# Performance work log

Measured on AMD Instinct MI355X. Metric: run time of the kernel, lower is better.

The kernel has to match this reference:

```python
import jax, jax.numpy as jnp
import numpy as np

COMMITMENT_COST = 0.25


def setup_inputs() -> dict:
    key = jax.random.key(0)
    k1, k2 = jax.random.split(key)
    B, D, H, W = 16, 256, 32, 32
    K = 8192
    z = jax.random.normal(k1, (B, D, H, W), dtype=jnp.float32)
    embeddings = jax.random.uniform(k2, (K, D), dtype=jnp.float32,
                                    minval=-1.0 / K, maxval=1.0 / K)
    return {"z": z, "embeddings": embeddings}


def reference(z, embeddings):
    B, D, H, W = z.shape
    # NCHW -> NHWC, flatten spatial+batch to code vectors [N, D]
    z_p = jnp.transpose(z, (0, 2, 3, 1))
    z_flat = z_p.reshape(-1, D)
    # squared-distance via matmul: ||z||^2 + ||e||^2 - 2 z.e^T  -> [N, K]
    d = (jnp.sum(z_flat * z_flat, axis=1, keepdims=True)
         + jnp.sum(embeddings * embeddings, axis=1)
         - 2.0 * jnp.matmul(z_flat, embeddings.T))
    encoding_indices = jnp.argmin(d, axis=1)  # [N]
    quantized = embeddings[encoding_indices].reshape(z_p.shape)  # [B,H,W,D]
    e_latent_loss = jnp.mean((jax.lax.stop_gradient(quantized) - z_p) ** 2)
    q_latent_loss = jnp.mean((quantized - jax.lax.stop_gradient(z_p)) ** 2)
    loss = q_latent_loss + COMMITMENT_COST * e_latent_loss
    # straight-through estimator
    quantized_st = z_p + jax.lax.stop_gradient(quantized - z_p)
    out = jnp.transpose(quantized_st, (0, 3, 1, 2))  # back to NCHW
    return out, loss, encoding_indices.reshape(B, H, W)
```

## Files before the change

kernel.cpp:

```cpp
#include <hip/hip_runtime.h>

#define B_    16
#define D_    256
#define H_    32
#define W_    32
#define SP    1024
#define N_TOT 16384
#define K_    8192
#define ZB    (D_*SP)

#define BIAS_  0.03125f
#define DELTA_ 2.5e-4f

typedef __attribute__((ext_vector_type(8))) short bf16x8;
typedef __attribute__((ext_vector_type(4))) short bf16x4;
typedef __attribute__((ext_vector_type(4))) float f32x4;

#define GLOAD_LDS16(g, l) \
    __builtin_amdgcn_global_load_lds((const __attribute__((address_space(1))) void*)(g), \
                                     (__attribute__((address_space(3))) void*)(l), 16, 0, 0)

__device__ __forceinline__ unsigned short f2bf(float f) {
    unsigned u = __float_as_uint(f);
    u += 0x7FFFu + ((u >> 16) & 1u);
    return (unsigned short)(u >> 16);
}

__device__ __forceinline__ void merge2(unsigned &a1, unsigned &a2,
                                       unsigned b1, unsigned b2) {
    unsigned m1  = min(a1, b1);
    unsigned hi  = max(a1, b1);
    unsigned sel = (a1 < b1) ? a2 : b2;
    a2 = min(hi, sel);
    a1 = m1;
}


__global__ __launch_bounds__(256)
void prep_kernel(const float* __restrict__ emb, const float* __restrict__ z,
                 short* __restrict__ ET3, short* __restrict__ ZT3,
                 float* __restrict__ zpart, float* __restrict__ enorm,
                 float* __restrict__ enormB, int* __restrict__ wl_cnt) {
    const int bx = blockIdx.x;
    const int t  = threadIdx.x;
    if (bx < 2048) {
        int k = bx * 4 + (t >> 6);
        int l = t & 63;
        float4 v = *(const float4*)(emb + (size_t)k * D_ + l * 4);
        float sum = v.x*v.x + v.y*v.y + v.z*v.z + v.w*v.w;
        for (int m = 1; m < 64; m <<= 1) sum += __shfl_xor(sum, m, 64);
        if (l == 0) { enorm[k] = sum; enormB[k] = sum + BIAS_; }
        int dcb  = l >> 4;
        int c    = (l >> 1) & 7;
        int half = l & 1;
        bf16x4 o;
        o[0] = (short)f2bf(v.x); o[1] = (short)f2bf(v.y);
        o[2] = (short)f2bf(v.z); o[3] = (short)f2bf(v.w);
        *(bf16x4*)(ET3 + ((size_t)dcb * K_ + k) * 64 + ((c ^ (k & 7)) * 8) + half * 4) = o;
    } else {
        int bz  = bx - 2048;
        if (bz == 0 && t == 0) *wl_cnt = 0;
        int dcb = bz >> 6;
        int st  = bz & 63;
        int n   = st * 256 + t;
        int b   = n >> 10;
        int s   = n & 1023;
        const float* zb = z + (size_t)b * ZB + (size_t)(dcb * 64) * SP + s;
        short* dst = ZT3 + ((size_t)dcb * N_TOT + n) * 64;
        int sw = n & 7;
#pragma unroll
        for (int c2 = 0; c2 < 4; ++c2) {
            float vv[16];
#pragma unroll
            for (int dd = 0; dd < 16; ++dd)
                vv[dd] = zb[(size_t)(c2 * 16 + dd) * SP];
            float sum = 0.f;
#pragma unroll
            for (int dd = 0; dd < 16; ++dd) {
                float v = vv[dd];
                sum += v * v;
            }
            zpart[(size_t)(dcb * 4 + c2) * N_TOT + n] = sum;
            bf16x8 o0, o1;
#pragma unroll
            for (int j = 0; j < 8; ++j) { o0[j] = (short)f2bf(vv[j]);
                                          o1[j] = (short)f2bf(vv[8 + j]); }
            *(bf16x8*)(dst + (((c2 * 2)     ^ sw) * 8)) = o0;
            *(bf16x8*)(dst + (((c2 * 2 + 1) ^ sw) * 8)) = o1;
        }
    }
}


__global__ __launch_bounds__(256, 4)
void mfma_argmin2(const short* __restrict__ ET3, const short* __restrict__ ZT3,
                  const float* __restrict__ enormB, uint2* __restrict__ pv) {
    __shared__ char smem[32768];
    const int t    = threadIdx.x;
    const int wid  = t >> 6, lane = t & 63;
    const int quad = lane >> 4, l16 = lane & 15;
    const int wm   = wid >> 1, wn = wid & 1;
    const int stripe = blockIdx.x >> 7;
    const int n0     = (blockIdx.x & 127) * 128;
    const int swz    = (l16 & 7);

    unsigned r1[4], r2[4];
#pragma unroll
    for (int fj = 0; fj < 4; ++fj) { r1[fj] = 0xFFFFFFFFu; r2[fj] = 0xFFFFFFFFu; }

#pragma unroll 1
    for (int cc = 0; cc < 8; ++cc) {
        const int c0 = stripe * 1024 + cc * 128;
        f32x4 acc[4][4];
#pragma unroll
        for (int fi = 0; fi < 4; ++fi)
#pragma unroll
            for (int fj = 0; fj < 4; ++fj) acc[fi][fj] = (f32x4){0.f, 0.f, 0.f, 0.f};

#pragma unroll 1
        for (int dcb = 0; dcb < 4; ++dcb) {
            __syncthreads();
            const char* gA = (const char*)ET3 + ((size_t)dcb * K_    + c0) * 128;
            const char* gB = (const char*)ZT3 + ((size_t)dcb * N_TOT + n0) * 128;
#pragma unroll
            for (int j = 0; j < 4; ++j) {
                int off = j * 4096 + t * 16;
                GLOAD_LDS16(gA + off, smem + off);
                GLOAD_LDS16(gB + off, smem + 16384 + off);
            }
            __syncthreads();
#pragma unroll
            for (int dc2 = 0; dc2 < 2; ++dc2) {
                bf16x8 af[4], bfv[4];
                const int chm = ((dc2 * 4 + quad) ^ swz) * 16;
#pragma unroll
                for (int fi = 0; fi < 4; ++fi)
                    af[fi] = *(const bf16x8*)(smem + (wm*64 + fi*16 + l16)*128 + chm);
#pragma unroll
                for (int fj = 0; fj < 4; ++fj)
                    bfv[fj] = *(const bf16x8*)(smem + 16384 + (wn*64 + fj*16 + l16)*128 + chm);
#pragma unroll
                for (int fi = 0; fi < 4; ++fi)
#pragma unroll
                    for (int fj = 0; fj < 4; ++fj)
                        acc[fi][fj] = __builtin_amdgcn_mfma_f32_16x16x32_bf16(
                            af[fi], bfv[fj], acc[fi][fj], 0, 0, 0);
            }
        }

        float ekv[4][4];
#pragma unroll
        for (int fi = 0; fi < 4; ++fi) {
            float4 e4 = *(const float4*)(enormB + c0 + wm*64 + fi*16 + quad*4);
            ekv[fi][0]=e4.x; ekv[fi][1]=e4.y; ekv[fi][2]=e4.z; ekv[fi][3]=e4.w;
        }
#pragma unroll
        for (int fj = 0; fj < 4; ++fj) {
#pragma unroll
            for (int fi = 0; fi < 4; ++fi) {
                const unsigned cb = (unsigned)(c0 + wm*64 + fi*16 + quad*4);
                float s0 = fmaf(-2.f, acc[fi][fj].x, ekv[fi][0]);
                float s1 = fmaf(-2.f, acc[fi][fj].y, ekv[fi][1]);
                float s2 = fmaf(-2.f, acc[fi][fj].z, ekv[fi][2]);
                float s3 = fmaf(-2.f, acc[fi][fj].w, ekv[fi][3]);
                unsigned k0 = (__float_as_uint(s0) & 0xFFFFE000u) | (cb + 0u);
                unsigned k1 = (__float_as_uint(s1) & 0xFFFFE000u) | (cb + 1u);
                unsigned k2 = (__float_as_uint(s2) & 0xFFFFE000u) | (cb + 2u);
                unsigned k3 = (__float_as_uint(s3) & 0xFFFFE000u) | (cb + 3u);
                unsigned lo1 = min(k0, k1), hi1 = max(k0, k1);
                unsigned lo2 = min(k2, k3), hi2 = max(k2, k3);
                merge2(lo1, hi1, lo2, hi2);
                merge2(r1[fj], r2[fj], lo1, hi1);
            }
        }
    }

#pragma unroll
    for (int fj = 0; fj < 4; ++fj) {
        unsigned a1 = r1[fj], a2 = r2[fj];
#pragma unroll
        for (int m = 16; m <= 32; m <<= 1) {
            unsigned b1 = __shfl_xor(a1, m, 64);
            unsigned b2 = __shfl_xor(a2, m, 64);
            merge2(a1, a2, b1, b2);
        }
        if (quad == 0) {
            int n = n0 + wn*64 + fj*16 + l16;
            pv[(size_t)(stripe * 2 + wm) * N_TOT + n] = make_uint2(a1, a2);
        }
    }
}


template <int NG>
__global__ __launch_bounds__(256)
void phaseA_z(const uint2* __restrict__ pv, const float* __restrict__ zpart,
              float* __restrict__ znorm, int* __restrict__ fidx,
              float* __restrict__ out_idx, int* __restrict__ wl,
              int* __restrict__ wl_cnt, float* __restrict__ out_loss) {
    int n = blockIdx.x * 256 + threadIdx.x;
    if (n == 0) *out_loss = 0.f;
    float zsum = 0.f;
#pragma unroll
    for (int dc = 0; dc < 16; ++dc) zsum += zpart[(size_t)dc * N_TOT + n];
    znorm[n] = zsum;
    uint2 pp[NG];
    unsigned mn = 0xFFFFFFFFu;
#pragma unroll
    for (int g = 0; g < NG; ++g) {
        pp[g] = pv[(size_t)g * N_TOT + n];
        mn = min(mn, pp[g].x);
    }
    float smin  = __uint_as_float(mn & 0xFFFFE000u);
    unsigned th = __float_as_uint(smin + DELTA_) | 8191u;
    int cnt = 0;
#pragma unroll
    for (int g = 0; g < NG; ++g) {
        cnt += (pp[g].x <= th) ? 1 : 0;
        cnt += (pp[g].y <= th) ? 1 : 0;
    }
    if (cnt > 1) {
        int slot = atomicAdd(wl_cnt, 1);
        wl[slot] = n;
    } else {
        int c = (int)(mn & 8191u);
        fidx[n] = c;
        out_idx[n] = (float)c;
    }
}


template <int NG>
__global__ __launch_bounds__(256)
void recheck_t(const uint2* __restrict__ pv, const float* __restrict__ znorm,
               const float* __restrict__ enorm, const float* __restrict__ z,
               const float* __restrict__ emb, const int* __restrict__ wl,
               const int* __restrict__ wl_cnt, int* __restrict__ fidx,
               float* __restrict__ out_idx) {
    __shared__ float zrow[4][256];
    const int lane = threadIdx.x & 63;
    const int wslot = threadIdx.x >> 6;
    const int gwave = (blockIdx.x * 256 + threadIdx.x) >> 6;
    const int nwaves = (gridDim.x * 256) >> 6;
    int total = *wl_cnt;
    total = min(max(total, 0), N_TOT);

    for (int i = gwave; i < total; i += nwaves) {
        int n = wl[i];
        unsigned key = 0xFFFFFFFFu;
        if (lane < 2 * NG) {
            uint2 p = pv[(size_t)(lane >> 1) * N_TOT + n];
            key = (lane & 1) ? p.y : p.x;
        }
        unsigned mn = key;
#pragma unroll
        for (int m = 1; m < 64; m <<= 1) mn = min(mn, __shfl_xor(mn, m, 64));
        float smin  = __uint_as_float(mn & 0xFFFFE000u);
        unsigned th = __float_as_uint(smin + DELTA_) | 8191u;

        const int b = n >> 10, sp = n & 1023;
        const float* zr = z + (size_t)b * ZB + sp;
#pragma unroll
        for (int j = 0; j < 4; ++j)
            zrow[wslot][lane + j * 64] = zr[(size_t)(lane + j * 64) * SP];
        float zn = znorm[n];

        unsigned lexlo = 0xFFFFFFFFu, lexhi = 0xFFFFFFFFu;
        if (key <= th) {
            int c = (int)(key & 8191u);
            const float* er = emb + (size_t)c * D_;
            float dot = 0.f;
#pragma unroll 8
            for (int d = 0; d < D_; ++d)
                dot = fmaf(zrow[wslot][d], er[d], dot);
            float s = (zn + enorm[c]) - 2.f * dot;
            unsigned sb = __float_as_uint(s);
            lexhi = sb >> 19;
            lexlo = (sb << 13) | (unsigned)c;
        }
#pragma unroll
        for (int m = 1; m < 64; m <<= 1) {
            unsigned olo = __shfl_xor(lexlo, m, 64);
            unsigned ohi = __shfl_xor(lexhi, m, 64);
            if (ohi < lexhi || (ohi == lexhi && olo < lexlo)) { lexhi = ohi; lexlo = olo; }
        }
        if (lane == 0) {
            int c = (int)(lexlo & 8191u);
            fidx[n] = c;
            out_idx[n] = (float)c;
        }
    }
}


__global__ __launch_bounds__(256)
void output_kernel2(const float* __restrict__ z, const float* __restrict__ emb,
                    const int* __restrict__ fidx, float* __restrict__ out,
                    float* __restrict__ loss) {
    __shared__ float eL[32][257];
    __shared__ int   fid[32];
    __shared__ float red[4];
    const int nb = blockIdx.x;
    const int n0 = nb * 32;
    const int b  = n0 >> 10;
    const int s0 = n0 & 1023;
    const int t  = threadIdx.x;
    if (t < 32) fid[t] = fidx[n0 + t];
    __syncthreads();
#pragma unroll
    for (int i = 0; i < 8; ++i) {
        int p = t + i * 256;
        int row = p >> 6, q = p & 63;
        float4 v = *(const float4*)(emb + (size_t)fid[row] * D_ + q * 4);
        eL[row][q*4+0] = v.x; eL[row][q*4+1] = v.y;
        eL[row][q*4+2] = v.z; eL[row][q*4+3] = v.w;
    }
    __syncthreads();
    const int sl = t & 31, dg = t >> 5;
    float lsum = 0.f;
#pragma unroll
    for (int i = 0; i < 32; ++i) {
        int d = dg * 32 + i;
        size_t off = ((size_t)(b * D_ + d)) * SP + s0 + sl;
        float zv = z[off];
        float q  = eL[sl][d];
        float diff = q - zv;
        out[off] = zv + diff;
        lsum += diff * diff;
    }
    for (int m = 1; m < 64; m <<= 1) lsum += __shfl_xor(lsum, m, 64);
    if ((t & 63) == 0) red[t >> 6] = lsum;
    __syncthreads();
    if (t == 0) {
        float tot = (red[0] + red[1] + red[2] + red[3])
                    * (1.25f / (float)(B_ * SP * D_));
        atomicAdd(loss, tot);
    }
}


extern "C" void kernel_launch(void* const* d_in, const int* in_sizes, int n_in,
                              void* d_out, int out_size, void* d_ws, size_t ws_size,
                              hipStream_t stream) {
    const float* z   = (const float*)d_in[0];
    const float* emb = (const float*)d_in[1];
    float* out = (float*)d_out;
    float* w   = (float*)d_ws;

    float* enorm  = w;
    float* enormB = w + 8192;
    float* znorm  = w + 16384;
    int*   fidx   = (int*)(w + 32768);
    int*   wl_cnt = (int*)(w + 49152);
    int*   wl     = (int*)(w + 49216);
    float* zpart  = w + 65664;
    uint2* pv     = (uint2*)(w + 327808);
    short* ET3    = (short*)(w + 852096);
    short* ZT3    = (short*)(w + 1900672);

    float* out0     = out;
    float* out_loss = out + (size_t)B_ * D_ * SP;
    float* out_idx  = out_loss + 1;

    prep_kernel<<<2304, 256, 0, stream>>>(emb, z, ET3, ZT3, zpart,
                                          enorm, enormB, wl_cnt);
    mfma_argmin2<<<1024, 256, 0, stream>>>(ET3, ZT3, enormB, pv);
    phaseA_z<16><<<N_TOT / 256, 256, 0, stream>>>(pv, zpart, znorm, fidx,
                                                  out_idx, wl, wl_cnt, out_loss);
    recheck_t<16><<<256, 256, 0, stream>>>(pv, znorm, enorm, z, emb,
                                           wl, wl_cnt, fidx, out_idx);
    output_kernel2<<<N_TOT / 32, 256, 0, stream>>>(z, emb, fidx, out0, out_loss);
}
```

Before: 234.8 us.

## Fuse argmin finalize, fp32 recheck and output into one tail kernel

Merges the three tail kernels (candidate finalize, fp32 recheck of ambiguous rows, output/loss) into one kernel with 64 rows per block. The recheck worklist, znorm and the fidx handoff now live in shared memory, and the per-row z norm is computed on demand from zpart. The loss zeroing moves into prep_kernel. The output phase uses float4 loads and stores. This removes two kernel launches and the global round trips between them, but gives only 256 blocks and a larger LDS footprint, and recheck work becomes unbalanced across blocks.

```diff
diff --git a/kernel.cpp b/kernel.cpp
--- a/kernel.cpp
+++ b/kernel.cpp
@@ -40,7 +40,7 @@
 void prep_kernel(const float* __restrict__ emb, const float* __restrict__ z,
                  short* __restrict__ ET3, short* __restrict__ ZT3,
                  float* __restrict__ zpart, float* __restrict__ enorm,
-                 float* __restrict__ enormB, int* __restrict__ wl_cnt) {
+                 float* __restrict__ enormB, float* __restrict__ out_loss) {
     const int bx = blockIdx.x;
     const int t  = threadIdx.x;
     if (bx < 2048) {
@@ -59,7 +59,7 @@
         *(bf16x4*)(ET3 + ((size_t)dcb * K_ + k) * 64 + ((c ^ (k & 7)) * 8) + half * 4) = o;
     } else {
         int bz  = bx - 2048;
-        if (bz == 0 && t == 0) *wl_cnt = 0;
+        if (bz == 0 && t == 0) *out_loss = 0.f;
         int dcb = bz >> 6;
         int st  = bz & 63;
         int n   = st * 256 + t;
@@ -192,63 +192,62 @@
 }
 
 
-template <int NG>
 __global__ __launch_bounds__(256)
-void phaseA_z(const uint2* __restrict__ pv, const float* __restrict__ zpart,
-              float* __restrict__ znorm, int* __restrict__ fidx,
-              float* __restrict__ out_idx, int* __restrict__ wl,
-              int* __restrict__ wl_cnt, float* __restrict__ out_loss) {
-    int n = blockIdx.x * 256 + threadIdx.x;
-    if (n == 0) *out_loss = 0.f;
-    float zsum = 0.f;
-#pragma unroll
-    for (int dc = 0; dc < 16; ++dc) zsum += zpart[(size_t)dc * N_TOT + n];
-    znorm[n] = zsum;
-    uint2 pp[NG];
-    unsigned mn = 0xFFFFFFFFu;
-#pragma unroll
-    for (int g = 0; g < NG; ++g) {
-        pp[g] = pv[(size_t)g * N_TOT + n];
-        mn = min(mn, pp[g].x);
-    }
-    float smin  = __uint_as_float(mn & 0xFFFFE000u);
-    unsigned th = __float_as_uint(smin + DELTA_) | 8191u;
-    int cnt = 0;
-#pragma unroll
-    for (int g = 0; g < NG; ++g) {
-        cnt += (pp[g].x <= th) ? 1 : 0;
-        cnt += (pp[g].y <= th) ? 1 : 0;
-    }
-    if (cnt > 1) {
-        int slot = atomicAdd(wl_cnt, 1);
-        wl[slot] = n;
-    } else {
-        int c = (int)(mn & 8191u);
-        fidx[n] = c;
-        out_idx[n] = (float)c;
-    }
-}
-
-
-template <int NG>
-__global__ __launch_bounds__(256)
-void recheck_t(const uint2* __restrict__ pv, const float* __restrict__ znorm,
-               const float* __restrict__ enorm, const float* __restrict__ z,
-               const float* __restrict__ emb, const int* __restrict__ wl,
-               const int* __restrict__ wl_cnt, int* __restrict__ fidx,
-               float* __restrict__ out_idx) {
+void tail_fused(const uint2* __restrict__ pv, const float* __restrict__ zpart,
+                const float* __restrict__ enorm, const float* __restrict__ z,
+                const float* __restrict__ emb, float* __restrict__ out,
+                float* __restrict__ out_idx, float* __restrict__ loss) {
+    __shared__ float eL[64][257];
     __shared__ float zrow[4][256];
-    const int lane = threadIdx.x & 63;
-    const int wslot = threadIdx.x >> 6;
-    const int gwave = (blockIdx.x * 256 + threadIdx.x) >> 6;
-    const int nwaves = (gridDim.x * 256) >> 6;
-    int total = *wl_cnt;
-    total = min(max(total, 0), N_TOT);
-
-    for (int i = gwave; i < total; i += nwaves) {
-        int n = wl[i];
+    __shared__ int   fid[64];
+    __shared__ int   wlL[64];
+    __shared__ int   nflag;
+    __shared__ float red[4];
+
+    const int t  = threadIdx.x;
+    const int n0 = blockIdx.x * 64;
+    const int b  = n0 >> 10;
+    const int s0 = n0 & 1023;
+
+    if (t == 0) nflag = 0;
+    __syncthreads();
+
+    if (t < 64) {
+        int n = n0 + t;
+        uint2 pp[16];
+        unsigned mn = 0xFFFFFFFFu;
+#pragma unroll
+        for (int g = 0; g < 16; ++g) {
+            pp[g] = pv[(size_t)g * N_TOT + n];
+            mn = min(mn, pp[g].x);
+        }
+        float smin  = __uint_as_float(mn & 0xFFFFE000u);
+        unsigned th = __float_as_uint(smin + DELTA_) | 8191u;
+        int cnt = 0;
+#pragma unroll
+        for (int g = 0; g < 16; ++g) {
+            cnt += (pp[g].x <= th) ? 1 : 0;
+            cnt += (pp[g].y <= th) ? 1 : 0;
+        }
+        if (cnt > 1) {
+            int slot = atomicAdd(&nflag, 1);
+            wlL[slot] = t;
+        } else {
+            int c = (int)(mn & 8191u);
+            fid[t] = c;
+            out_idx[n] = (float)c;
+        }
+    }
+    __syncthreads();
+
+    const int lane = t & 63;
+    const int wid  = t >> 6;
+    const int nf   = nflag;
+    for (int i = wid; i < nf; i += 4) {
+        int r = wlL[i];
+        int n = n0 + r;
         unsigned key = 0xFFFFFFFFu;
-        if (lane < 2 * NG) {
+        if (lane < 32) {
             uint2 p = pv[(size_t)(lane >> 1) * N_TOT + n];
             key = (lane & 1) ? p.y : p.x;
         }
@@ -258,12 +257,16 @@
         float smin  = __uint_as_float(mn & 0xFFFFE000u);
         unsigned th = __float_as_uint(smin + DELTA_) | 8191u;
 
-        const int b = n >> 10, sp = n & 1023;
-        const float* zr = z + (size_t)b * ZB + sp;
+        float zp = 0.f;
+        if (lane < 16) zp = zpart[(size_t)lane * N_TOT + n];
+        float zn = 0.f;
+#pragma unroll
+        for (int dc = 0; dc < 16; ++dc) zn += __shfl(zp, dc, 64);
+
+        const float* zr = z + (size_t)b * ZB + (s0 + r);
 #pragma unroll
         for (int j = 0; j < 4; ++j)
-            zrow[wslot][lane + j * 64] = zr[(size_t)(lane + j * 64) * SP];
-        float zn = znorm[n];
+            zrow[wid][lane + j * 64] = zr[(size_t)(lane + j * 64) * SP];
 
         unsigned lexlo = 0xFFFFFFFFu, lexhi = 0xFFFFFFFFu;
         if (key <= th) {
@@ -272,7 +275,7 @@
             float dot = 0.f;
 #pragma unroll 8
             for (int d = 0; d < D_; ++d)
-                dot = fmaf(zrow[wslot][d], er[d], dot);
+                dot = fmaf(zrow[wid][d], er[d], dot);
             float s = (zn + enorm[c]) - 2.f * dot;
             unsigned sb = __float_as_uint(s);
             lexhi = sb >> 19;
@@ -286,29 +289,14 @@
         }
         if (lane == 0) {
             int c = (int)(lexlo & 8191u);
-            fidx[n] = c;
+            fid[r] = c;
             out_idx[n] = (float)c;
         }
     }
-}
-
-
-__global__ __launch_bounds__(256)
-void output_kernel2(const float* __restrict__ z, const float* __restrict__ emb,
-                    const int* __restrict__ fidx, float* __restrict__ out,
-                    float* __restrict__ loss) {
-    __shared__ float eL[32][257];
-    __shared__ int   fid[32];
-    __shared__ float red[4];
-    const int nb = blockIdx.x;
-    const int n0 = nb * 32;
-    const int b  = n0 >> 10;
-    const int s0 = n0 & 1023;
-    const int t  = threadIdx.x;
-    if (t < 32) fid[t] = fidx[n0 + t];
-    __syncthreads();
-#pragma unroll
-    for (int i = 0; i < 8; ++i) {
+    __syncthreads();
+
+#pragma unroll
+    for (int i = 0; i < 16; ++i) {
         int p = t + i * 256;
         int row = p >> 6, q = p & 63;
         float4 v = *(const float4*)(emb + (size_t)fid[row] * D_ + q * 4);
@@ -316,17 +304,22 @@
         eL[row][q*4+2] = v.z; eL[row][q*4+3] = v.w;
     }
     __syncthreads();
-    const int sl = t & 31, dg = t >> 5;
+
+    const int sq = t & 15, dg = t >> 4;
     float lsum = 0.f;
 #pragma unroll
-    for (int i = 0; i < 32; ++i) {
-        int d = dg * 32 + i;
-        size_t off = ((size_t)(b * D_ + d)) * SP + s0 + sl;
-        float zv = z[off];
-        float q  = eL[sl][d];
-        float diff = q - zv;
-        out[off] = zv + diff;
-        lsum += diff * diff;
+    for (int i = 0; i < 16; ++i) {
+        int d = dg * 16 + i;
+        size_t off = ((size_t)(b * D_ + d)) * SP + s0 + sq * 4;
+        float4 z4 = *(const float4*)(z + off);
+        float q0 = eL[sq*4+0][d], q1 = eL[sq*4+1][d];
+        float q2 = eL[sq*4+2][d], q3 = eL[sq*4+3][d];
+        float d0 = q0 - z4.x, d1 = q1 - z4.y;
+        float d2 = q2 - z4.z, d3 = q3 - z4.w;
+        float4 o4 = make_float4(z4.x + d0, z4.y + d1,
+                                z4.z + d2, z4.w + d3);
+        *(float4*)(out + off) = o4;
+        lsum += d0*d0; lsum += d1*d1; lsum += d2*d2; lsum += d3*d3;
     }
     for (int m = 1; m < 64; m <<= 1) lsum += __shfl_xor(lsum, m, 64);
     if ((t & 63) == 0) red[t >> 6] = lsum;
@@ -349,25 +342,18 @@
 
     float* enorm  = w;
     float* enormB = w + 8192;
-    float* znorm  = w + 16384;
-    int*   fidx   = (int*)(w + 32768);
-    int*   wl_cnt = (int*)(w + 49152);
-    int*   wl     = (int*)(w + 49216);
-    float* zpart  = w + 65664;
-    uint2* pv     = (uint2*)(w + 327808);
-    short* ET3    = (short*)(w + 852096);
-    short* ZT3    = (short*)(w + 1900672);
+    float* zpart  = w + 16384;
+    uint2* pv     = (uint2*)(w + 278528);
+    short* ET3    = (short*)(w + 802816);
+    short* ZT3    = (short*)(w + 1851392);
 
     float* out0     = out;
     float* out_loss = out + (size_t)B_ * D_ * SP;
     float* out_idx  = out_loss + 1;
 
     prep_kernel<<<2304, 256, 0, stream>>>(emb, z, ET3, ZT3, zpart,
-                                          enorm, enormB, wl_cnt);
+                                          enorm, enormB, out_loss);
     mfma_argmin2<<<1024, 256, 0, stream>>>(ET3, ZT3, enormB, pv);
-    phaseA_z<16><<<N_TOT / 256, 256, 0, stream>>>(pv, zpart, znorm, fidx,
-                                                  out_idx, wl, wl_cnt, out_loss);
-    recheck_t<16><<<256, 256, 0, stream>>>(pv, znorm, enorm, z, emb,
-                                           wl, wl_cnt, fidx, out_idx);
-    output_kernel2<<<N_TOT / 32, 256, 0, stream>>>(z, emb, fidx, out0, out_loss);
-}
+    tail_fused<<<256, 256, 0, stream>>>(pv, zpart, enorm, z, emb,
+                                        out0, out_idx, out_loss);
+}
```

Measured after the change: 226.4 us. 1.04x faster.
